# Optimization experiments

Measured on AMD Instinct MI355X. Metric: run time of the kernel, lower is better.

The kernel has to match this reference:

```python
import jax, jax.numpy as jnp
import numpy as np

TEMPERATURE = 0.1
NORM_EPS = 1e-12  # torch F.normalize clamps the norm at 1e-12


def _l2_normalize(x):
    n = jnp.sqrt(jnp.sum(x * x, axis=-1, keepdims=True))
    return x / jnp.maximum(n, NORM_EPS)


def setup_inputs() -> dict:
    key = jax.random.key(0)
    k1, k2 = jax.random.split(key)
    feat = jax.random.normal(k1, (32, 384, 28, 28), dtype=jnp.float32)
    codebook = jax.random.normal(k2, (2048, 384), dtype=jnp.float32)
    return {"feat": feat, "codebook": codebook}


def reference(feat, codebook):
    # feat: (b, c, h, w); codebook: (K, c)
    b, c, h, w = feat.shape
    K = codebook.shape[0]

    f = jnp.transpose(feat, (0, 2, 3, 1))          # (b, h, w, c), unnormalized
    flat = f.reshape(-1, c)                        # (N, c)
    flat_n = _l2_normalize(flat)                   # normalize=True
    code = _l2_normalize(codebook)                 # (K, c)

    distance = (jnp.sum(flat_n * flat_n, axis=1, keepdims=True)
                + jnp.sum(code * code, axis=1)
                - 2.0 * (flat_n @ code.T))

    # hard assignment (is_weight_sum=False): gather nearest code
    idx = jnp.argmin(distance, axis=1)             # (N,)
    q = code[idx]                                  # (N, c) == one_hot(idx) @ code
    q = q.reshape(b, h, w, c)

    # straight-through: gradient flows to f, not the quantized values
    q_feat = f + jax.lax.stop_gradient(q - f)      # (b, h, w, c)
    q_feat = jnp.transpose(q_feat, (0, 3, 1, 2))   # (b, c, h, w)

    prob = jax.nn.softmax(-distance / TEMPERATURE, axis=1)  # (N, K)
    assignment = jnp.transpose(prob.reshape(b, h, w, K), (0, 3, 1, 2))  # (b, K, h, w)

    return (f, q_feat, assignment, distance)
```

## Files before the change

kernel.cpp:

```cpp
#include <hip/hip_runtime.h>

#define B_  32
#define C_  384
#define HW_ 784
#define N_  25088
#define K_  2048
#define PPX 112

#define OFF_F    0
#define OFF_Q    9633792
#define OFF_ASG  19267584
#define OFF_DIST 70647808

#define MARGIN 0.02f

typedef unsigned short u16;
typedef unsigned int u32;
typedef __attribute__((ext_vector_type(8))) short short8;
typedef __attribute__((ext_vector_type(4))) float floatx4;
typedef __attribute__((ext_vector_type(4))) float f32x4;
typedef __attribute__((ext_vector_type(4))) u16 u16x4;
typedef __attribute__((ext_vector_type(8))) u16 u16x8;

static __device__ __forceinline__ u16 f2bf(float x) {
    u32 u = __builtin_bit_cast(u32, x);
    u32 r = (u + 0x7FFFu + ((u >> 16) & 1u)) >> 16;
    return (u16)r;
}
static __device__ __forceinline__ float bf2f(u16 v) {
    return __builtin_bit_cast(float, (u32)v << 16);
}

static __device__ __forceinline__ void gload_lds16(const void* g, void* l) {
    __builtin_amdgcn_global_load_lds(
        (const __attribute__((address_space(1))) unsigned int*)g,
        (__attribute__((address_space(3))) unsigned int*)l,
        16, 0, 0);
}

static __device__ __forceinline__ size_t qslot(int b, int s, int hw) {
    return ((size_t)b * C_ + s) * HW_ + hw;
}

__global__ __launch_bounds__(256) void k_prep(const float* __restrict__ feat,
                                              const float* __restrict__ cb,
                                              float* __restrict__ f_out,
                                              float* __restrict__ inv_n,
                                              u16* __restrict__ a_hi,
                                              float* __restrict__ code_n,
                                              u16* __restrict__ b_hi) {
    int tid = threadIdx.x;
    if (blockIdx.x >= 1568) {
        int row  = (blockIdx.x - 1568) * 4 + (tid >> 6);
        int lane = tid & 63;
        const float* src = cb + (size_t)row * C_;
        float v[6];
        float ss = 0.f;
#pragma unroll
        for (int i = 0; i < 6; ++i) { v[i] = src[lane + 64 * i]; ss += v[i] * v[i]; }
#pragma unroll
        for (int off = 32; off; off >>= 1) ss += __shfl_xor(ss, off, 64);
        float inv = 1.f / fmaxf(sqrtf(ss), 1e-12f);
#pragma unroll
        for (int i = 0; i < 6; ++i) {
            float vn = v[i] * inv;
            code_n[(size_t)row * C_ + lane + 64 * i] = vn;
            b_hi  [(size_t)row * C_ + lane + 64 * i] = f2bf(vn);
        }
        return;
    }
    __shared__ float tile[C_][17];
    __shared__ float red[16][17];
    __shared__ float s_inv[16];
    int b   = blockIdx.x / 49;
    int hw0 = (blockIdx.x - b * 49) * 16;
    int px  = tid & 15, cq = tid >> 4;

#pragma unroll
    for (int it = 0; it < 24; ++it) {
        int c = cq + 16 * it;
        tile[c][px] = feat[((size_t)(b * C_ + c)) * HW_ + hw0 + px];
    }
    __syncthreads();
    float ss = 0.f;
#pragma unroll
    for (int q = 0; q < 24; ++q) {
        float v = tile[cq + 16 * q][px];
        ss = fmaf(v, v, ss);
    }
    red[cq][px] = ss;
    __syncthreads();
    if (tid < 16) {
        float tot = 0.f;
#pragma unroll
        for (int p = 0; p < 16; ++p) tot += red[p][tid];
        float inv = 1.f / fmaxf(sqrtf(tot), 1e-12f);
        s_inv[tid] = inv;
        inv_n[(size_t)b * HW_ + hw0 + tid] = inv;
    }
    __syncthreads();

    {
        int p2 = tid >> 4, cc = tid & 15;
        float* fb = f_out + ((size_t)(b * HW_ + hw0 + p2)) * C_;
#pragma unroll
        for (int it = 0; it < 6; ++it) {
            int c0 = cc * 4 + 64 * it;
            f32x4 v;
            v[0] = tile[c0 + 0][p2];
            v[1] = tile[c0 + 1][p2];
            v[2] = tile[c0 + 2][p2];
            v[3] = tile[c0 + 3][p2];
            __builtin_nontemporal_store(v, (f32x4*)(fb + c0));
        }
    }
    {
        int p2 = tid >> 4, cc = tid & 15;
        float inv = s_inv[p2];
        u16* aptr = a_hi + ((size_t)(b * HW_ + hw0 + p2)) * C_;
#pragma unroll
        for (int it = 0; it < 12; ++it) {
            int c0 = 2 * cc + 32 * it;
            u16 h0 = f2bf(tile[c0][p2] * inv);
            u16 h1 = f2bf(tile[c0 + 1][p2] * inv);
            *(u32*)(aptr + c0) = (u32)h0 | ((u32)h1 << 16);
        }
    }
}

template <bool DB>
__global__ __launch_bounds__(256) void k_gemm(const u16* __restrict__ A,
                                              const u16* __restrict__ Bm,
                                              float* __restrict__ D,
                                              u16* __restrict__ db) {
    __shared__ u16 As[2][128 * 32];
    __shared__ u16 Bs[2][128 * 32];
    int tid = threadIdx.x;
    int lin = blockIdx.x;
    int swz = (lin & 7) * 392 + (lin >> 3);
    int n0 = (swz & 15) * 128;
    int m0 = (swz >> 4) * 128;
    int w = tid >> 6, l = tid & 63;
    int wm = (w >> 1) * 64, wn = (w & 1) * 64;
    int q4 = l >> 4, r15 = l & 15;

    floatx4 acc[4][4];
#pragma unroll
    for (int i = 0; i < 4; ++i)
#pragma unroll
        for (int j = 0; j < 4; ++j) acc[i][j] = (floatx4)0.f;

    int srow = tid >> 2;
    int sp   = tid & 3;
    int fs   = (srow ^ (srow >> 2)) & 3;
    int kk0  = 8 * (sp ^ fs);

#define STAGE(buf, kt)                                                          \
    {                                                                           \
        _Pragma("unroll")                                                       \
        for (int q = 0; q < 2; ++q) {                                           \
            int row = q * 64 + srow;                                            \
            int off = (q * 256 + tid) * 16;                                     \
            gload_lds16(A  + (size_t)(m0 + row) * C_ + (kt) + kk0,              \
                        (char*)As[buf] + off);                                  \
            gload_lds16(Bm + (size_t)(n0 + row) * C_ + (kt) + kk0,              \
                        (char*)Bs[buf] + off);                                  \
        }                                                                       \
    }

    STAGE(0, 0);
    __syncthreads();

    const int slot = (q4 ^ ((r15 ^ (r15 >> 2)) & 3)) << 4;
#pragma unroll 1
    for (int t = 0; t < 12; ++t) {
        int cur = t & 1;
        if (t < 11) STAGE(cur ^ 1, (t + 1) * 32);
        const char* Ab = (const char*)As[cur];
        const char* Bb = (const char*)Bs[cur];
        short8 a[4], b[4];
#pragma unroll
        for (int i = 0; i < 4; ++i) {
            a[i] = *(const short8*)(Ab + (wm + i * 16 + r15) * 64 + slot);
            b[i] = *(const short8*)(Bb + (wn + i * 16 + r15) * 64 + slot);
        }
#pragma unroll
        for (int i = 0; i < 4; ++i)
#pragma unroll
            for (int j = 0; j < 4; ++j)
                acc[i][j] = __builtin_amdgcn_mfma_f32_16x16x32_bf16(a[i], b[j], acc[i][j], 0, 0, 0);
        __syncthreads();
    }

#pragma unroll
    for (int i = 0; i < 4; ++i) {
        int gm = m0 + wm + i * 16 + q4 * 4;
#pragma unroll
        for (int j = 0; j < 4; ++j) {
            int gn = n0 + wn + j * 16 + r15;
#pragma unroll
            for (int r = 0; r < 4; ++r) {
                float d = 2.f - 2.f * acc[i][j][r];
                if (DB) {
                    __builtin_nontemporal_store(d, D + (size_t)(gm + r) * K_ + gn);
                    db[(size_t)(gm + r) * K_ + gn] = f2bf(d);
                } else {
                    D[(size_t)(gm + r) * K_ + gn] = d;
                }
            }
        }
    }
#undef STAGE
}

__global__ __launch_bounds__(256) void k_stats_b(const u16* __restrict__ db,
                                                 float2* __restrict__ srow) {
    int row = blockIdx.x * 4 + (threadIdx.x >> 6);
    int l   = threadIdx.x & 63;
    const u16* dr = db + (size_t)row * K_;
    float es = 0.f, dm = 3.4e38f;
#pragma unroll
    for (int i = 0; i < 4; ++i) {
        u16x8 v = *(const u16x8*)(dr + l * 8 + 512 * i);
#pragma unroll
        for (int e = 0; e < 8; ++e) {
            float d = bf2f(v[e]);
            es += __expf(-10.f * d);
            dm = fminf(dm, d);
        }
    }
#pragma unroll
    for (int off = 32; off; off >>= 1) {
        es += __shfl_xor(es, off, 64);
        dm = fminf(dm, __shfl_xor(dm, off, 64));
    }
    if (l == 0) {
        float2 st;
        st.x = 1.f / es;
        st.y = dm + MARGIN;
        srow[row] = st;
    }
}

__global__ __launch_bounds__(256) void k_stats_f(const float* __restrict__ D,
                                                 float2* __restrict__ srow) {
    int row = blockIdx.x * 4 + (threadIdx.x >> 6);
    int l   = threadIdx.x & 63;
    const float* dr = D + (size_t)row * K_;
    float es = 0.f, dm = 3.4e38f;
#pragma unroll
    for (int i = 0; i < 8; ++i) {
        float4 v = *(const float4*)(dr + l * 4 + 256 * i);
        es += __expf(-10.f * v.x) + __expf(-10.f * v.y)
            + __expf(-10.f * v.z) + __expf(-10.f * v.w);
        dm = fminf(dm, fminf(fminf(v.x, v.y), fminf(v.z, v.w)));
    }
#pragma unroll
    for (int off = 32; off; off >>= 1) {
        es += __shfl_xor(es, off, 64);
        dm = fminf(dm, __shfl_xor(dm, off, 64));
    }
    if (l == 0) {
        float2 st;
        st.x = 1.f / es;
        st.y = dm + MARGIN;
        srow[row] = st;
    }
}

__global__ __launch_bounds__(256) void k_post_b(const u16* __restrict__ db,
                                                const float2* __restrict__ srow,
                                                u32* __restrict__ Qi,
                                                float* __restrict__ asg) {
    __shared__ float tbuf[64][113];
    __shared__ float s_inv[PPX], s_thr[PPX];
    __shared__ int   s_cnt[PPX];
    __shared__ int   s_cand[PPX][16];
    int tile = blockIdx.x;
    int kc   = blockIdx.y;
    int b    = tile / 7;
    int hw0  = (tile - b * 7) * PPX;
    int n0   = b * HW_ + hw0;
    int tid  = threadIdx.x;

    if (tid < PPX) {
        float2 st = srow[n0 + tid];
        s_inv[tid] = st.x;
        s_thr[tid] = st.y;
        s_cnt[tid] = 0;
    }
    __syncthreads();

    int r16 = tid >> 4, c4 = (tid & 15) * 4;
    int px = tid & 127, kg = tid >> 7;
#pragma unroll 1
    for (int ch = 0; ch < 8; ++ch) {
        int k0 = kc * 512 + ch * 64;
#pragma unroll
        for (int rr = 0; rr < 7; ++rr) {
            int row = r16 + 16 * rr;
            u16x4 dv = *(const u16x4*)(db + (size_t)(n0 + row) * K_ + k0 + c4);
            float inv = s_inv[row], thr = s_thr[row];
#pragma unroll
            for (int cc = 0; cc < 4; ++cc) {
                float d = bf2f(dv[cc]);
                tbuf[c4 + cc][row] = __expf(-10.f * d) * inv;
                if (d <= thr) {
                    int idx = atomicAdd(&s_cnt[row], 1);
                    if (idx < 16) s_cand[row][idx] = k0 + c4 + cc;
                }
            }
        }
        __syncthreads();
        if (px < PPX) {
            size_t base = ((size_t)(b * K_ + k0 + kg * 32)) * HW_ + hw0 + px;
#pragma unroll
            for (int ki = 0; ki < 32; ++ki)
                __builtin_nontemporal_store(tbuf[kg * 32 + ki][px],
                                            asg + base + (size_t)ki * HW_);
        }
        __syncthreads();
    }

    if (tid < PPX) {
        int cnt = s_cnt[tid];
        cnt = cnt > 16 ? 16 : cnt;
        Qi[qslot(b, kc * 17, hw0 + tid)] = (u32)cnt;
        for (int ci = 0; ci < cnt; ++ci)
            Qi[qslot(b, kc * 17 + 1 + ci, hw0 + tid)] = (u32)s_cand[tid][ci];
    }
}

__global__ __launch_bounds__(256) void k_post_f(const float* __restrict__ D,
                                                const float2* __restrict__ srow,
                                                u32* __restrict__ Qi,
                                                float* __restrict__ asg) {
    __shared__ float tbuf[64][113];
    __shared__ float s_inv[PPX], s_thr[PPX];
    __shared__ int   s_cnt[PPX];
    __shared__ int   s_cand[PPX][16];
    int tile = blockIdx.x;
    int kc   = blockIdx.y;
    int b    = tile / 7;
    int hw0  = (tile - b * 7) * PPX;
    int n0   = b * HW_ + hw0;
    int tid  = threadIdx.x;

    if (tid < PPX) {
        float2 st = srow[n0 + tid];
        s_inv[tid] = st.x;
        s_thr[tid] = st.y;
        s_cnt[tid] = 0;
    }
    __syncthreads();

    int r16 = tid >> 4, c4 = (tid & 15) * 4;
    int px = tid & 127, kg = tid >> 7;
#pragma unroll 1
    for (int ch = 0; ch < 8; ++ch) {
        int k0 = kc * 512 + ch * 64;
#pragma unroll
        for (int rr = 0; rr < 7; ++rr) {
            int row = r16 + 16 * rr;
            f32x4 dv = __builtin_nontemporal_load(
                (const f32x4*)(D + (size_t)(n0 + row) * K_ + k0 + c4));
            float inv = s_inv[row], thr = s_thr[row];
#pragma unroll
            for (int cc = 0; cc < 4; ++cc) {
                float d = dv[cc];
                tbuf[c4 + cc][row] = __expf(-10.f * d) * inv;
                if (d <= thr) {
                    int idx = atomicAdd(&s_cnt[row], 1);
                    if (idx < 16) s_cand[row][idx] = k0 + c4 + cc;
                }
            }
        }
        __syncthreads();
        if (px < PPX) {
            size_t base = ((size_t)(b * K_ + k0 + kg * 32)) * HW_ + hw0 + px;
#pragma unroll
            for (int ki = 0; ki < 32; ++ki)
                __builtin_nontemporal_store(tbuf[kg * 32 + ki][px],
                                            asg + base + (size_t)ki * HW_);
        }
        __syncthreads();
    }

    if (tid < PPX) {
        int cnt = s_cnt[tid];
        cnt = cnt > 16 ? 16 : cnt;
        Qi[qslot(b, kc * 17, hw0 + tid)] = (u32)cnt;
        for (int ci = 0; ci < cnt; ++ci)
            Qi[qslot(b, kc * 17 + 1 + ci, hw0 + tid)] = (u32)s_cand[tid][ci];
    }
}

__global__ __launch_bounds__(256) void k_q(const u32* __restrict__ Qi,
                                           const float* __restrict__ codeN,
                                           const float* __restrict__ invN,
                                           const float* __restrict__ f_in,
                                           float* __restrict__ qOut) {
    __shared__ int s_amin[PPX], s_cnt[PPX];
    __shared__ int s_cand[PPX][64];
    int tile = blockIdx.x;
    int b    = tile / 7;
    int hw0  = (tile - b * 7) * PPX;
    int npix = b * HW_ + hw0;
    int tid  = threadIdx.x;

    if (tid < PPX) {
        int total = 0;
#pragma unroll
        for (int kc = 0; kc < 4; ++kc) {
            int cnt = (int)Qi[qslot(b, kc * 17, hw0 + tid)];
            for (int ci = 0; ci < cnt; ++ci)
                s_cand[tid][total++] = (int)Qi[qslot(b, kc * 17 + 1 + ci, hw0 + tid)];
        }
        s_cnt[tid]  = total;
        s_amin[tid] = s_cand[tid][0];
    }
    __syncthreads();

    int w = tid >> 6, l = tid & 63;
#pragma unroll 1
    for (int r = w; r < PPX; r += 4) {
        int cnt = s_cnt[r];
        if (cnt < 2) continue;
        float ivn = invN[npix + r];
        float fv[6];
        const float* frow = f_in + (size_t)(npix + r) * C_;
#pragma unroll
        for (int ii = 0; ii < 6; ++ii)
            fv[ii] = frow[l + 64 * ii] * ivn;
        float dbest = 3.4e38f;
        int   kbest = -1;
        for (int ci = 0; ci < cnt; ++ci) {
            int k = s_cand[r][ci];
            float dt = 0.f;
            const float* cr = codeN + (size_t)k * C_;
#pragma unroll
            for (int ii = 0; ii < 6; ++ii) dt = fmaf(fv[ii], cr[l + 64 * ii], dt);
#pragma unroll
            for (int off = 1; off < 64; off <<= 1) dt += __shfl_xor(dt, off, 64);
            float dex = 2.f - 2.f * dt;
            if (kbest < 0 || dex < dbest || (dex == dbest && k < kbest)) { dbest = dex; kbest = k; }
        }
        if (l == 0) s_amin[r] = kbest;
    }
    __syncthreads();

    int px = tid & 127, kg = tid >> 7;
    if (px < PPX) {
        const float* cr = codeN + (size_t)s_amin[px] * C_ + kg * 192;
        size_t qb = ((size_t)b * C_ + kg * 192) * HW_ + hw0 + px;
#pragma unroll 1
        for (int c4 = 0; c4 < 48; ++c4) {
            float4 v = *(const float4*)(cr + 4 * c4);
            __builtin_nontemporal_store(v.x, qOut + qb + (size_t)(4 * c4 + 0) * HW_);
            __builtin_nontemporal_store(v.y, qOut + qb + (size_t)(4 * c4 + 1) * HW_);
            __builtin_nontemporal_store(v.z, qOut + qb + (size_t)(4 * c4 + 2) * HW_);
            __builtin_nontemporal_store(v.w, qOut + qb + (size_t)(4 * c4 + 3) * HW_);
        }
    }
}

extern "C" void kernel_launch(void* const* d_in, const int* in_sizes, int n_in,
                              void* d_out, int out_size, void* d_ws, size_t ws_size,
                              hipStream_t stream) {
    const float* feat = (const float*)d_in[0];
    const float* cb   = (const float*)d_in[1];
    float* out    = (float*)d_out;
    float* f_out  = out + OFF_F;
    float* q_out  = out + OFF_Q;
    float* asg    = out + OFF_ASG;
    float* dist   = out + OFF_DIST;

    u16* a_hi = (u16*)asg;
    u16* b_hi = a_hi + (size_t)N_ * C_;
    u32* Qi   = (u32*)q_out;

    const size_t DB_BYTES = (size_t)N_ * K_ * 2;
    bool big = ws_size >= DB_BYTES + 3145728 + 100352 + 200704;

    if (big) {
        u16*    db     = (u16*)d_ws;
        float*  code_n = (float*)((char*)d_ws + DB_BYTES);
        float*  inv_n  = (float*)((char*)d_ws + DB_BYTES + 3145728);
        float2* srow   = (float2*)((char*)d_ws + DB_BYTES + 3145728 + 100352);

        k_prep<<<2080, 256, 0, stream>>>(feat, cb, f_out, inv_n, a_hi, code_n, b_hi);
        k_gemm<true><<<3136, 256, 0, stream>>>(a_hi, b_hi, dist, db);
        k_stats_b<<<N_ / 4, 256, 0, stream>>>(db, srow);
        k_post_b<<<dim3(224, 4), 256, 0, stream>>>(db, srow, Qi, asg);
        k_q<<<224, 256, 0, stream>>>(Qi, code_n, inv_n, f_out, q_out);
    } else {
        float*  code_n = (float*)d_ws;
        float*  inv_n  = (float*)((char*)d_ws + 3145728);
        float2* srow   = (float2*)((char*)d_ws + 3246080);

        k_prep<<<2080, 256, 0, stream>>>(feat, cb, f_out, inv_n, a_hi, code_n, b_hi);
        k_gemm<false><<<3136, 256, 0, stream>>>(a_hi, b_hi, dist, nullptr);
        k_stats_f<<<N_ / 4, 256, 0, stream>>>(dist, srow);
        k_post_f<<<dim3(224, 4), 256, 0, stream>>>(dist, srow, Qi, asg);
        k_q<<<224, 256, 0, stream>>>(Qi, code_n, inv_n, f_out, q_out);
    }
}
```

Measured before the change: 247.0 us.

## Fuse row stats, softmax post-pass and codeword gather into one kernel

```diff
diff --git a/kernel.cpp b/kernel.cpp
--- a/kernel.cpp
+++ b/kernel.cpp
@@ -213,89 +213,56 @@
 #undef STAGE
 }
 
-__global__ __launch_bounds__(256) void k_stats_b(const u16* __restrict__ db,
-                                                 float2* __restrict__ srow) {
-    int row = blockIdx.x * 4 + (threadIdx.x >> 6);
-    int l   = threadIdx.x & 63;
-    const u16* dr = db + (size_t)row * K_;
-    float es = 0.f, dm = 3.4e38f;
-#pragma unroll
-    for (int i = 0; i < 4; ++i) {
-        u16x8 v = *(const u16x8*)(dr + l * 8 + 512 * i);
-#pragma unroll
-        for (int e = 0; e < 8; ++e) {
-            float d = bf2f(v[e]);
-            es += __expf(-10.f * d);
-            dm = fminf(dm, d);
-        }
-    }
-#pragma unroll
-    for (int off = 32; off; off >>= 1) {
-        es += __shfl_xor(es, off, 64);
-        dm = fminf(dm, __shfl_xor(dm, off, 64));
-    }
-    if (l == 0) {
-        float2 st;
-        st.x = 1.f / es;
-        st.y = dm + MARGIN;
-        srow[row] = st;
-    }
-}
-
-__global__ __launch_bounds__(256) void k_stats_f(const float* __restrict__ D,
-                                                 float2* __restrict__ srow) {
-    int row = blockIdx.x * 4 + (threadIdx.x >> 6);
-    int l   = threadIdx.x & 63;
-    const float* dr = D + (size_t)row * K_;
-    float es = 0.f, dm = 3.4e38f;
-#pragma unroll
-    for (int i = 0; i < 8; ++i) {
-        float4 v = *(const float4*)(dr + l * 4 + 256 * i);
-        es += __expf(-10.f * v.x) + __expf(-10.f * v.y)
-            + __expf(-10.f * v.z) + __expf(-10.f * v.w);
-        dm = fminf(dm, fminf(fminf(v.x, v.y), fminf(v.z, v.w)));
-    }
-#pragma unroll
-    for (int off = 32; off; off >>= 1) {
-        es += __shfl_xor(es, off, 64);
-        dm = fminf(dm, __shfl_xor(dm, off, 64));
-    }
-    if (l == 0) {
-        float2 st;
-        st.x = 1.f / es;
-        st.y = dm + MARGIN;
-        srow[row] = st;
-    }
-}
-
-__global__ __launch_bounds__(256) void k_post_b(const u16* __restrict__ db,
-                                                const float2* __restrict__ srow,
-                                                u32* __restrict__ Qi,
-                                                float* __restrict__ asg) {
+__global__ __launch_bounds__(256) void k_fin(const u16* __restrict__ db,
+                                             const float* __restrict__ codeN,
+                                             const float* __restrict__ invN,
+                                             const float* __restrict__ f_in,
+                                             float* __restrict__ asg,
+                                             float* __restrict__ qOut) {
     __shared__ float tbuf[64][113];
     __shared__ float s_inv[PPX], s_thr[PPX];
-    __shared__ int   s_cnt[PPX];
+    __shared__ int   s_cnt[PPX], s_amin[PPX];
     __shared__ int   s_cand[PPX][16];
     int tile = blockIdx.x;
-    int kc   = blockIdx.y;
     int b    = tile / 7;
     int hw0  = (tile - b * 7) * PPX;
     int n0   = b * HW_ + hw0;
     int tid  = threadIdx.x;
-
-    if (tid < PPX) {
-        float2 st = srow[n0 + tid];
-        s_inv[tid] = st.x;
-        s_thr[tid] = st.y;
-        s_cnt[tid] = 0;
+    int w = tid >> 6, l = tid & 63;
+
+    if (tid < PPX) s_cnt[tid] = 0;
+
+#pragma unroll 1
+    for (int r = w; r < PPX; r += 4) {
+        const u16* dr = db + (size_t)(n0 + r) * K_;
+        float es = 0.f, dm = 3.4e38f;
+#pragma unroll
+        for (int i = 0; i < 4; ++i) {
+            u16x8 v = *(const u16x8*)(dr + l * 8 + 512 * i);
+#pragma unroll
+            for (int e = 0; e < 8; ++e) {
+                float d = bf2f(v[e]);
+                es += __expf(-10.f * d);
+                dm = fminf(dm, d);
+            }
+        }
+#pragma unroll
+        for (int off = 32; off; off >>= 1) {
+            es += __shfl_xor(es, off, 64);
+            dm = fminf(dm, __shfl_xor(dm, off, 64));
+        }
+        if (l == 0) {
+            s_inv[r] = 1.f / es;
+            s_thr[r] = dm + MARGIN;
+        }
     }
     __syncthreads();
 
     int r16 = tid >> 4, c4 = (tid & 15) * 4;
     int px = tid & 127, kg = tid >> 7;
 #pragma unroll 1
-    for (int ch = 0; ch < 8; ++ch) {
-        int k0 = kc * 512 + ch * 64;
+    for (int ch = 0; ch < 32; ++ch) {
+        int k0 = ch * 64;
 #pragma unroll
         for (int rr = 0; rr < 7; ++rr) {
             int row = r16 + 16 * rr;
@@ -322,12 +289,74 @@
         __syncthreads();
     }
 
-    if (tid < PPX) {
-        int cnt = s_cnt[tid];
+    if (tid < PPX) s_amin[tid] = s_cand[tid][0];
+    __syncthreads();
+
+#pragma unroll 1
+    for (int r = w; r < PPX; r += 4) {
+        int cnt = s_cnt[r];
+        if (cnt < 2) continue;
         cnt = cnt > 16 ? 16 : cnt;
-        Qi[qslot(b, kc * 17, hw0 + tid)] = (u32)cnt;
-        for (int ci = 0; ci < cnt; ++ci)
-            Qi[qslot(b, kc * 17 + 1 + ci, hw0 + tid)] = (u32)s_cand[tid][ci];
+        float ivn = invN[n0 + r];
+        float fv[6];
+        const float* frow = f_in + (size_t)(n0 + r) * C_;
+#pragma unroll
+        for (int ii = 0; ii < 6; ++ii)
+            fv[ii] = frow[l + 64 * ii] * ivn;
+        float dbest = 3.4e38f;
+        int   kbest = -1;
+        for (int ci = 0; ci < cnt; ++ci) {
+            int k = s_cand[r][ci];
+            float dt = 0.f;
+            const float* cr = codeN + (size_t)k * C_;
+#pragma unroll
+            for (int ii = 0; ii < 6; ++ii) dt = fmaf(fv[ii], cr[l + 64 * ii], dt);
+#pragma unroll
+            for (int off = 1; off < 64; off <<= 1) dt += __shfl_xor(dt, off, 64);
+            float dex = 2.f - 2.f * dt;
+            if (kbest < 0 || dex < dbest || (dex == dbest && k < kbest)) { dbest = dex; kbest = k; }
+        }
+        if (l == 0) s_amin[r] = kbest;
+    }
+    __syncthreads();
+
+    if (px < PPX) {
+        const float* cr = codeN + (size_t)s_amin[px] * C_ + kg * 192;
+        size_t qb = ((size_t)b * C_ + kg * 192) * HW_ + hw0 + px;
+#pragma unroll 1
+        for (int c4i = 0; c4i < 48; ++c4i) {
+            float4 v = *(const float4*)(cr + 4 * c4i);
+            __builtin_nontemporal_store(v.x, qOut + qb + (size_t)(4 * c4i + 0) * HW_);
+            __builtin_nontemporal_store(v.y, qOut + qb + (size_t)(4 * c4i + 1) * HW_);
+            __builtin_nontemporal_store(v.z, qOut + qb + (size_t)(4 * c4i + 2) * HW_);
+            __builtin_nontemporal_store(v.w, qOut + qb + (size_t)(4 * c4i + 3) * HW_);
+        }
+    }
+}
+
+__global__ __launch_bounds__(256) void k_stats_f(const float* __restrict__ D,
+                                                 float2* __restrict__ srow) {
+    int row = blockIdx.x * 4 + (threadIdx.x >> 6);
+    int l   = threadIdx.x & 63;
+    const float* dr = D + (size_t)row * K_;
+    float es = 0.f, dm = 3.4e38f;
+#pragma unroll
+    for (int i = 0; i < 8; ++i) {
+        float4 v = *(const float4*)(dr + l * 4 + 256 * i);
+        es += __expf(-10.f * v.x) + __expf(-10.f * v.y)
+            + __expf(-10.f * v.z) + __expf(-10.f * v.w);
+        dm = fminf(dm, fminf(fminf(v.x, v.y), fminf(v.z, v.w)));
+    }
+#pragma unroll
+    for (int off = 32; off; off >>= 1) {
+        es += __shfl_xor(es, off, 64);
+        dm = fminf(dm, __shfl_xor(dm, off, 64));
+    }
+    if (l == 0) {
+        float2 st;
+        st.x = 1.f / es;
+        st.y = dm + MARGIN;
+        srow[row] = st;
     }
 }
 
@@ -477,7 +506,6 @@
 
     u16* a_hi = (u16*)asg;
     u16* b_hi = a_hi + (size_t)N_ * C_;
-    u32* Qi   = (u32*)q_out;
 
     const size_t DB_BYTES = (size_t)N_ * K_ * 2;
     bool big = ws_size >= DB_BYTES + 3145728 + 100352 + 200704;
@@ -486,17 +514,15 @@
         u16*    db     = (u16*)d_ws;
         float*  code_n = (float*)((char*)d_ws + DB_BYTES);
         float*  inv_n  = (float*)((char*)d_ws + DB_BYTES + 3145728);
-        float2* srow   = (float2*)((char*)d_ws + DB_BYTES + 3145728 + 100352);
 
         k_prep<<<2080, 256, 0, stream>>>(feat, cb, f_out, inv_n, a_hi, code_n, b_hi);
         k_gemm<true><<<3136, 256, 0, stream>>>(a_hi, b_hi, dist, db);
-        k_stats_b<<<N_ / 4, 256, 0, stream>>>(db, srow);
-        k_post_b<<<dim3(224, 4), 256, 0, stream>>>(db, srow, Qi, asg);
-        k_q<<<224, 256, 0, stream>>>(Qi, code_n, inv_n, f_out, q_out);
+        k_fin<<<224, 256, 0, stream>>>(db, code_n, inv_n, f_out, asg, q_out);
     } else {
         float*  code_n = (float*)d_ws;
         float*  inv_n  = (float*)((char*)d_ws + 3145728);
         float2* srow   = (float2*)((char*)d_ws + 3246080);
+        u32*    Qi     = (u32*)q_out;
 
         k_prep<<<2080, 256, 0, stream>>>(feat, cb, f_out, inv_n, a_hi, code_n, b_hi);
         k_gemm<false><<<3136, 256, 0, stream>>>(a_hi, b_hi, dist, nullptr);
```

Measured after the change: 321.3 us. 30.1% more time.
